# Kernel optimization log

Hardware: AMD Instinct MI355X
Metric: run time of the kernel (lower is better)

The kernel has to match this reference:

```python
import jax, jax.numpy as jnp
import numpy as np

T, D, H, N = 2048, 2048, 32, 64
DW, DA, DV, DG = 64, 64, 32, 128


def _ln(x, w, b, eps):
    mu = x.mean(-1, keepdims=True)
    var = ((x - mu) ** 2).mean(-1, keepdims=True)
    return (x - mu) * jax.lax.rsqrt(var + eps) * w + b


def setup_inputs() -> dict:
    key = jax.random.key(0)
    ks = iter(jax.random.split(key, 40))

    def rn(shape, s=0.02):
        return jax.random.normal(next(ks), shape, dtype=jnp.float32) * s

    def ru(shape):
        return jax.random.uniform(next(ks), shape, dtype=jnp.float32)

    return dict(
        x=rn((T, D), 1.0),
        state1=rn((1, D), 1.0),
        state2=rn((H, N, N), 0.1),
        v_first=rn((T, D), 1.0),
        ln1_w=jnp.ones((D,), jnp.float32),
        ln1_b=jnp.zeros((D,), jnp.float32),
        x_r=ru((D,)), x_w=ru((D,)), x_k=ru((D,)),
        x_v=ru((D,)), x_a=ru((D,)), x_g=ru((D,)),
        W_r=rn((D, D)), W_k=rn((D, D)), W_v=rn((D, D)), W_o=rn((D, D)),
        w1=rn((D, DW)), w2=rn((DW, D)), w0=rn((D,), 0.5),
        a1=rn((D, DA)), a2=rn((DA, D)), a0=rn((D,), 0.5),
        v1=rn((D, DV)), v2=rn((DV, D)), v0=rn((D,), 0.5),
        g1=rn((D, DG)), g2=rn((DG, D)),
        k_k=rn((D,), 0.5), k_a=rn((D,), 0.5), r_k=rn((D,), 0.5),
        ln_x_w=jnp.ones((D,), jnp.float32),
        ln_x_b=jnp.zeros((D,), jnp.float32),
    )


def reference(x, state1, state2, v_first, ln1_w, ln1_b,
              x_r, x_w, x_k, x_v, x_a, x_g,
              W_r, W_k, W_v, W_o,
              w1, w2, w0, a1, a2, a0, v1, v2, v0, g1, g2,
              k_k, k_a, r_k, ln_x_w, ln_x_b):
    # ln1 + token shift
    xn = _ln(x, ln1_w, ln1_b, 1e-5)                      # [T, D]
    sx = jnp.concatenate([state1, xn[:-1]], axis=0) - xn  # shifted - x
    xr = xn + sx * x_r
    xw = xn + sx * x_w
    xk = xn + sx * x_k
    xv = xn + sx * x_v
    xa = xn + sx * x_a
    xg = xn + sx * x_g

    r = xr @ W_r.T
    # decay: w = exp(-0.606531 * sigmoid(w0 + tanh(xw@w1)@w2))
    w = jnp.exp(-0.606531 * jax.nn.sigmoid(jnp.tanh(xw @ w1) @ w2 + w0))
    k = xk @ W_k.T
    v = xv @ W_v.T
    a = jax.nn.sigmoid(xa @ a1 @ a2 + a0)
    g = jax.nn.sigmoid(xg @ g1) @ g2
    # layer_id != 0: blend with v_first via v-lora
    v = v + (v_first - v) * jax.nn.sigmoid(xv @ v1 @ v2 + v0)

    kh = (k * k_k).reshape(T, H, N)
    kk = kh / (jnp.linalg.norm(kh, axis=-1, keepdims=True) + 1e-6)  # l2norm per head
    k = k * (1.0 + (a - 1.0) * k_a)

    rh = r.reshape(T, H, N)
    wh = w.reshape(T, H, N)
    khh = k.reshape(T, H, N)
    vh = v.reshape(T, H, N)
    ab = kk * a.reshape(T, H, N)  # b input to wkv

    def step(S, t):
        r_t, w_t, k_t, v_t, kk_t, ab_t = t
        sa = jnp.einsum('hij,hj->hi', S, -kk_t)  # state @ a (a = -kk column)
        S = (S * w_t[:, None, :]
             + sa[:, :, None] * ab_t[:, None, :]
             + v_t[:, :, None] * k_t[:, None, :])
        return S, jnp.einsum('hij,hj->hi', S, r_t)

    state2_out, xo = jax.lax.scan(step, state2, (rh, wh, khh, vh, kk, ab))  # xo: [T,H,N]

    # per-head layernorm (ln_x, eps=0.00064), then full-width affine
    xo = _ln(xo, jnp.float32(1.0), jnp.float32(0.0), 0.00064)
    xo = xo.reshape(T, D) * ln_x_w + ln_x_b
    # r_k bonus term
    bonus = ((rh * khh * r_k.reshape(H, N)).sum(-1, keepdims=True) * vh).reshape(T, D)
    xo = (xo + bonus) * g
    out = x + xo @ W_o.T
    return out, xn[-1:], state2_out
```

## Files before the change

### kernel.cpp

```cpp
#include <hip/hip_runtime.h>

#define Tn 2048
#define Dn 2048
#define Hn 32
#define Cn 32
#define NCH (Tn / Cn)

typedef float f32x4 __attribute__((ext_vector_type(4)));
typedef __bf16 bf16x8 __attribute__((ext_vector_type(8)));
typedef __bf16 bf16x4 __attribute__((ext_vector_type(4)));

template <int CTRL>
__device__ __forceinline__ float dpp_add(float x) {
  int xi = __builtin_bit_cast(int, x);
  int sh = __builtin_amdgcn_update_dpp(0, xi, CTRL, 0xf, 0xf, true);
  return x + __builtin_bit_cast(float, sh);
}
__device__ __forceinline__ float rdlane(float x, int l) {
  int xi = __builtin_bit_cast(int, x);
  return __builtin_bit_cast(float, __builtin_amdgcn_readlane(xi, l));
}
__device__ __forceinline__ float waveSum(float v) {
  v = dpp_add<0x111>(v);
  v = dpp_add<0x112>(v);
  v = dpp_add<0x114>(v);
  v = dpp_add<0x118>(v);
  return (rdlane(v, 15) + rdlane(v, 31)) + (rdlane(v, 47) + rdlane(v, 63));
}

__device__ __forceinline__ float sigm(float x) { return 1.f / (1.f + expf(-x)); }

__device__ __forceinline__ void gl_lds16(const void* g, void* l) {
  __builtin_amdgcn_global_load_lds(
      (__attribute__((address_space(1))) void*)(g),
      (__attribute__((address_space(3))) void*)(l), 16, 0, 0);
}

__device__ __forceinline__ void bar_lgkm() {
  asm volatile("s_waitcnt lgkmcnt(0)" ::: "memory");
  __builtin_amdgcn_s_barrier();
}

__device__ __forceinline__ f32x4 mfma16(const __bf16* a, const __bf16* b, f32x4 acc) {
  return __builtin_amdgcn_mfma_f32_16x16x32_bf16(
      *(const bf16x8*)a, *(const bf16x8*)b, acc, 0, 0, 0);
}


__global__ __launch_bounds__(256) void castw3_kernel(
    const float* __restrict__ A, const float* __restrict__ B,
    const float* __restrict__ C, __bf16* __restrict__ o0,
    __bf16* __restrict__ o1, __bf16* __restrict__ o2) {
  const int z = blockIdx.y;
  const float* src = z == 0 ? A : (z == 1 ? B : C);
  __bf16* dst = z == 0 ? o0 : (z == 1 ? o1 : o2);
  const size_t i4 = (size_t)blockIdx.x * 256 + threadIdx.x;
  f32x4 v = *(const f32x4*)(src + i4 * 4);
  bf16x4 o;
  o[0] = (__bf16)v[0]; o[1] = (__bf16)v[1]; o[2] = (__bf16)v[2]; o[3] = (__bf16)v[3];
  ((bf16x4*)dst)[i4] = o;
}

__global__ __launch_bounds__(256) void cast1_kernel(
    const float* __restrict__ src, __bf16* __restrict__ dst) {
  const size_t i4 = (size_t)blockIdx.x * 256 + threadIdx.x;
  f32x4 v = *(const f32x4*)(src + i4 * 4);
  bf16x4 o;
  o[0] = (__bf16)v[0]; o[1] = (__bf16)v[1]; o[2] = (__bf16)v[2]; o[3] = (__bf16)v[3];
  ((bf16x4*)dst)[i4] = o;
}

__global__ __launch_bounds__(256) void castT_kernel(
    const float* __restrict__ w2, const float* __restrict__ a2,
    const float* __restrict__ v2, const float* __restrict__ g2,
    __bf16* __restrict__ w2T, __bf16* __restrict__ a2T,
    __bf16* __restrict__ v2T, __bf16* __restrict__ g2T) {
  const int i = blockIdx.x;
  const int k = threadIdx.x;
  if (k < 128) {
    w2T[(size_t)i * 128 + k] = (k < 64) ? (__bf16)w2[(size_t)k * Dn + i] : (__bf16)0.f;
    a2T[(size_t)i * 128 + k] = (k < 64) ? (__bf16)a2[(size_t)k * Dn + i] : (__bf16)0.f;
    v2T[(size_t)i * 128 + k] = (k < 32) ? (__bf16)v2[(size_t)k * Dn + i] : (__bf16)0.f;
    g2T[(size_t)i * 128 + k] = (__bf16)g2[(size_t)k * Dn + i];
  }
}

__global__ __launch_bounds__(256) void castU_kernel(
    const float* __restrict__ w1, const float* __restrict__ a1,
    const float* __restrict__ v1, const float* __restrict__ g1,
    __bf16* __restrict__ uwT, __bf16* __restrict__ uaT,
    __bf16* __restrict__ uvT, __bf16* __restrict__ ugT) {
  const int z = blockIdx.y;
  const float* src = z == 0 ? w1 : (z == 1 ? a1 : (z == 2 ? v1 : g1));
  __bf16* dst = z == 0 ? uwT : (z == 1 ? uaT : (z == 2 ? uvT : ugT));
  const int R = z == 0 ? 64 : (z == 1 ? 64 : (z == 2 ? 32 : 128));
  const int d = blockIdx.x;
  const int k = threadIdx.x;
  if (k < 128)
    dst[(size_t)k * Dn + d] = (k < R) ? (__bf16)src[(size_t)d * R + k] : (__bf16)0.f;
}


__global__ __launch_bounds__(256) void ln_kernel(
    const float* __restrict__ x, const float* __restrict__ lw,
    const float* __restrict__ lb, __bf16* __restrict__ xn,
    float* __restrict__ xn_last) {
  __shared__ float red[8];
  const int t = blockIdx.x, tid = threadIdx.x;
  const int lane = tid & 63, wv = tid >> 6;
  const float* xr = x + (size_t)t * Dn;
  float v[8];
  float s = 0.f;
#pragma unroll
  for (int c = 0; c < 8; ++c) { v[c] = xr[tid + c * 256]; s += v[c]; }
  s = waveSum(s);
  if (lane == 0) red[wv] = s;
  __syncthreads();
  const float mu = (red[0] + red[1] + red[2] + red[3]) * (1.f / (float)Dn);
  float q = 0.f;
#pragma unroll
  for (int c = 0; c < 8; ++c) { float d0 = v[c] - mu; q += d0 * d0; }
  q = waveSum(q);
  if (lane == 0) red[4 + wv] = q;
  __syncthreads();
  const float var = (red[4] + red[5] + red[6] + red[7]) * (1.f / (float)Dn);
  const float rstd = rsqrtf(var + 1e-5f);
#pragma unroll
  for (int c = 0; c < 8; ++c) {
    const int d = tid + c * 256;
    const float y = (v[c] - mu) * rstd * lw[d] + lb[d];
    xn[(size_t)t * Dn + d] = (__bf16)y;
    if (t == Tn - 1) xn_last[d] = y;
  }
}


__global__ __launch_bounds__(256) void mix_kernel(
    const __bf16* __restrict__ xn, const float* __restrict__ state1,
    const float* __restrict__ cr, const float* __restrict__ cw,
    const float* __restrict__ ck, const float* __restrict__ cv,
    const float* __restrict__ ca, const float* __restrict__ cg,
    __bf16* __restrict__ br, __bf16* __restrict__ bw, __bf16* __restrict__ bk,
    __bf16* __restrict__ bv, __bf16* __restrict__ ba, __bf16* __restrict__ bg) {
  const size_t i4 = (size_t)blockIdx.x * 256 + threadIdx.x;
  const int t = (int)(i4 >> 9);
  const int d = (int)(i4 & 511) * 4;
  const bf16x4 cb = ((const bf16x4*)xn)[i4];
  f32x4 cur;
#pragma unroll
  for (int e = 0; e < 4; ++e) cur[e] = (float)cb[e];
  f32x4 prv;
  if (t == 0) {
    prv = *(const f32x4*)(state1 + d);
  } else {
    const bf16x4 pb = ((const bf16x4*)xn)[i4 - 512];
#pragma unroll
    for (int e = 0; e < 4; ++e) prv[e] = (float)pb[e];
  }
  const f32x4 sx = prv - cur;
  auto mix1 = [&](const float* c, __bf16* o) {
    const f32x4 cc = *(const f32x4*)(c + d);
    bf16x4 ob;
#pragma unroll
    for (int e = 0; e < 4; ++e) ob[e] = (__bf16)(cur[e] + sx[e] * cc[e]);
    ((bf16x4*)o)[i4] = ob;
  };
  mix1(cr, br); mix1(cw, bw); mix1(ck, bk);
  mix1(cv, bv); mix1(ca, ba); mix1(cg, bg);
}


__device__ __forceinline__ void gemm_tile(const __bf16* __restrict__ A,
                                          const __bf16* __restrict__ B,
                                          int K, int row0, int col0,
                                          f32x4 (&acc)[4][4]) {
  __shared__ __attribute__((aligned(16))) __bf16 As[4096];
  __shared__ __attribute__((aligned(16))) __bf16 Bs[4096];
  const int tid = threadIdx.x;
  const int lane = tid & 63, wid = tid >> 6;
  const int wm = (wid >> 1) * 64, wn = (wid & 1) * 64;
  const int lr = lane & 15, lk = (lane >> 4) * 8;
  for (int kt = 0; kt < K; kt += 32) {
#pragma unroll
    for (int it = 0; it < 2; ++it) {
      const int L = it * 256 + tid;
      const int rr = L >> 2, kc = (L & 3) * 8;
      const int lb = (it * 256 + wid * 64) * 8;
      gl_lds16(A + (size_t)(row0 + rr) * K + (kt + kc), &As[lb]);
      gl_lds16(B + (size_t)(col0 + rr) * K + (kt + kc), &Bs[lb]);
    }
    __syncthreads();
    bf16x8 af[4], bfv[4];
#pragma unroll
    for (int mf = 0; mf < 4; ++mf)
      af[mf] = *(const bf16x8*)&As[(wm + mf * 16 + lr) * 32 + lk];
#pragma unroll
    for (int nf = 0; nf < 4; ++nf)
      bfv[nf] = *(const bf16x8*)&Bs[(wn + nf * 16 + lr) * 32 + lk];
#pragma unroll
    for (int mf = 0; mf < 4; ++mf)
#pragma unroll
      for (int nf = 0; nf < 4; ++nf)
        acc[mf][nf] = __builtin_amdgcn_mfma_f32_16x16x32_bf16(
            af[mf], bfv[nf], acc[mf][nf], 0, 0, 0);
    __syncthreads();
  }
}

__global__ __launch_bounds__(256) void gemm3_kernel(
    const __bf16* __restrict__ A0, const __bf16* __restrict__ A1,
    const __bf16* __restrict__ A2, const __bf16* __restrict__ B0,
    const __bf16* __restrict__ B1, const __bf16* __restrict__ B2,
    __bf16* __restrict__ C0, __bf16* __restrict__ C1, __bf16* __restrict__ C2) {
  const int z = blockIdx.z;
  const __bf16* A = z == 0 ? A0 : (z == 1 ? A1 : A2);
  const __bf16* B = z == 0 ? B0 : (z == 1 ? B1 : B2);
  __bf16* C = z == 0 ? C0 : (z == 1 ? C1 : C2);
  const int row0 = blockIdx.x * 128, col0 = blockIdx.y * 128;
  f32x4 acc[4][4] = {};
  gemm_tile(A, B, Dn, row0, col0, acc);
  const int lane = threadIdx.x & 63, wid = threadIdx.x >> 6;
  const int wm = (wid >> 1) * 64, wn = (wid & 1) * 64;
#pragma unroll
  for (int mf = 0; mf < 4; ++mf) {
    const int r0 = row0 + wm + mf * 16 + ((lane >> 4) << 2);
#pragma unroll
    for (int nf = 0; nf < 4; ++nf) {
      const int c0 = col0 + wn + nf * 16 + (lane & 15);
#pragma unroll
      for (int rg = 0; rg < 4; ++rg)
        C[(size_t)(r0 + rg) * Dn + c0] = (__bf16)acc[mf][nf][rg];
    }
  }
}

__global__ __launch_bounds__(256) void gemm_l1_kernel(
    const __bf16* __restrict__ Aw, const __bf16* __restrict__ Aa,
    const __bf16* __restrict__ Av, const __bf16* __restrict__ Ag,
    const __bf16* __restrict__ Bw, const __bf16* __restrict__ Ba,
    const __bf16* __restrict__ Bv, const __bf16* __restrict__ Bg,
    __bf16* __restrict__ Cw, __bf16* __restrict__ Ca,
    __bf16* __restrict__ Cv, __bf16* __restrict__ Cg) {
  const int z = blockIdx.z;
  const __bf16* A = z == 0 ? Aw : (z == 1 ? Aa : (z == 2 ? Av : Ag));
  const __bf16* B = z == 0 ? Bw : (z == 1 ? Ba : (z == 2 ? Bv : Bg));
  __bf16* C = z == 0 ? Cw : (z == 1 ? Ca : (z == 2 ? Cv : Cg));
  const int row0 = blockIdx.x * 128;
  f32x4 acc[4][4] = {};
  gemm_tile(A, B, Dn, row0, 0, acc);
  const int lane = threadIdx.x & 63, wid = threadIdx.x >> 6;
  const int wm = (wid >> 1) * 64, wn = (wid & 1) * 64;
#pragma unroll
  for (int mf = 0; mf < 4; ++mf) {
    const int r0 = row0 + wm + mf * 16 + ((lane >> 4) << 2);
#pragma unroll
    for (int nf = 0; nf < 4; ++nf) {
      const int c0 = wn + nf * 16 + (lane & 15);
#pragma unroll
      for (int rg = 0; rg < 4; ++rg) {
        float val = acc[mf][nf][rg];
        if (z == 0)      val = tanhf(val);
        else if (z == 3) val = sigm(val);
        C[(size_t)(r0 + rg) * 128 + c0] = (__bf16)val;
      }
    }
  }
}

__global__ __launch_bounds__(256) void gemm_s2_kernel(
    const __bf16* __restrict__ Aw, const __bf16* __restrict__ Aa,
    const __bf16* __restrict__ Av, const __bf16* __restrict__ Ag,
    const __bf16* __restrict__ Bw, const __bf16* __restrict__ Ba,
    const __bf16* __restrict__ Bv, const __bf16* __restrict__ Bg,
    const float* __restrict__ w0, const float* __restrict__ a0,
    const float* __restrict__ v0, __bf16* __restrict__ Cw,
    __bf16* __restrict__ Ca, __bf16* __restrict__ Cv, __bf16* __restrict__ Cg) {
  const int z = blockIdx.z;
  const __bf16* A = z == 0 ? Aw : (z == 1 ? Aa : (z == 2 ? Av : Ag));
  const __bf16* B = z == 0 ? Bw : (z == 1 ? Ba : (z == 2 ? Bv : Bg));
  const float* bias = z == 0 ? w0 : (z == 1 ? a0 : (z == 2 ? v0 : (const float*)0));
  __bf16* C = z == 0 ? Cw : (z == 1 ? Ca : (z == 2 ? Cv : Cg));
  const int row0 = blockIdx.x * 128, col0 = blockIdx.y * 128;
  f32x4 acc[4][4] = {};
  gemm_tile(A, B, 128, row0, col0, acc);
  const int lane = threadIdx.x & 63, wid = threadIdx.x >> 6;
  const int wm = (wid >> 1) * 64, wn = (wid & 1) * 64;
#pragma unroll
  for (int mf = 0; mf < 4; ++mf) {
    const int r0 = row0 + wm + mf * 16 + ((lane >> 4) << 2);
#pragma unroll
    for (int nf = 0; nf < 4; ++nf) {
      const int c0 = col0 + wn + nf * 16 + (lane & 15);
#pragma unroll
      for (int rg = 0; rg < 4; ++rg) {
        float val = acc[mf][nf][rg];
        if (z == 0)      val = expf(-0.606531f * sigm(val + bias[c0]));
        else if (z < 3)  val = sigm(val + bias[c0]);
        C[(size_t)(r0 + rg) * Dn + c0] = (__bf16)val;
      }
    }
  }
}

__global__ __launch_bounds__(256) void gemm_wo_kernel(
    const __bf16* __restrict__ A, const __bf16* __restrict__ B,
    const float* __restrict__ xres, float* __restrict__ C) {
  const int row0 = blockIdx.x * 128, col0 = blockIdx.y * 128;
  f32x4 acc[4][4] = {};
  gemm_tile(A, B, Dn, row0, col0, acc);
  const int lane = threadIdx.x & 63, wid = threadIdx.x >> 6;
  const int wm = (wid >> 1) * 64, wn = (wid & 1) * 64;
#pragma unroll
  for (int mf = 0; mf < 4; ++mf) {
    const int r0 = row0 + wm + mf * 16 + ((lane >> 4) << 2);
#pragma unroll
    for (int nf = 0; nf < 4; ++nf) {
      const int c0 = col0 + wn + nf * 16 + (lane & 15);
#pragma unroll
      for (int rg = 0; rg < 4; ++rg)
        C[(size_t)(r0 + rg) * Dn + c0] =
            acc[mf][nf][rg] + xres[(size_t)(r0 + rg) * Dn + c0];
    }
  }
}


__global__ __launch_bounds__(256) void prep_kernel(
    const __bf16* __restrict__ r, __bf16* __restrict__ k, __bf16* __restrict__ v,
    const __bf16* __restrict__ a, const __bf16* __restrict__ vb,
    const float* __restrict__ v_first, const float* __restrict__ k_k,
    const float* __restrict__ k_a, const float* __restrict__ r_k,
    __bf16* __restrict__ kk_out, __bf16* __restrict__ ab_out,
    float* __restrict__ dot_out) {
  const int t = blockIdx.x;
  const int lane = threadIdx.x & 63, wv = threadIdx.x >> 6;
#pragma unroll 1
  for (int c = 0; c < 8; ++c) {
    const int d = c * 256 + wv * 64 + lane;
    const size_t idx = (size_t)t * Dn + d;
    const float kvv = (float)k[idx];
    const float kh = kvv * k_k[d];
    const float nrm = sqrtf(waveSum(kh * kh)) + 1e-6f;
    const float kkv = kh / nrm;
    const float av = (float)a[idx];
    float vv = (float)v[idx];
    vv = vv + (v_first[idx] - vv) * (float)vb[idx];
    const float kfv = kvv * (1.f + (av - 1.f) * k_a[d]);
    const float dt = waveSum((float)r[idx] * kfv * r_k[d]);
    kk_out[idx] = (__bf16)kkv;
    ab_out[idx] = (__bf16)(kkv * av);
    k[idx] = (__bf16)kfv;
    v[idx] = (__bf16)vv;
    if (lane == 0) dot_out[t * Hn + (d >> 6)] = dt;
  }
}


__global__ __launch_bounds__(256) void chunkA_kernel(
    const __bf16* __restrict__ wd, const __bf16* __restrict__ kk,
    const __bf16* __restrict__ ab, const __bf16* __restrict__ kf,
    const __bf16* __restrict__ r,
    __bf16* __restrict__ Atil, __bf16* __restrict__ Rtil,
    __bf16* __restrict__ BhatT, __bf16* __restrict__ KhatT,
    __bf16* __restrict__ Pg, __bf16* __restrict__ PKg,
    __bf16* __restrict__ Gbg, __bf16* __restrict__ Gkg,
    float* __restrict__ WCg) {
  const int c = blockIdx.x, h = blockIdx.y;
  const int tid = threadIdx.x;
  __shared__ __bf16 A_l[32][72];
  __shared__ __bf16 B_l[32][72], K_l[32][72], R_l[32][72];
  __shared__ float W_l[33][64];
  __shared__ float Mba[32][36], Mka[32][36];
  __shared__ float P0[32][36], P1[32][36], T0[32][36], T1[32][36];

  const size_t rowbase = (size_t)(c * Cn) * Dn + (size_t)h * 64;
  const int tt = tid >> 3, j0 = (tid & 7) * 8;
  const size_t g = rowbase + (size_t)tt * Dn + j0;
  *(bf16x8*)&A_l[tt][j0] = *(const bf16x8*)(wd + g);
  __syncthreads();
  if (tid < 64) {
    const int j = tid;
    float cur = 1.f;
    W_l[0][j] = 1.f;
    for (int t = 0; t < Cn; ++t) {
      cur *= (float)A_l[t][j];
      W_l[t + 1][j] = cur;
    }
    WCg[((size_t)c * Hn + h) * 64 + j] = cur;
  }
  __syncthreads();
  {
    bf16x8 kkv = *(const bf16x8*)(kk + g);
    bf16x8 abv = *(const bf16x8*)(ab + g);
    bf16x8 kv  = *(const bf16x8*)(kf + g);
    bf16x8 rv  = *(const bf16x8*)(r + g);
    bf16x8 oa, ob, ok, orr;
    const size_t tb = ((size_t)c * Hn + h) * 2048;
#pragma unroll
    for (int e = 0; e < 8; ++e) {
      const int j = j0 + e;
      const float Wexc = W_l[tt][j], Winc = W_l[tt + 1][j], WC = W_l[32][j];
      const float inv = 1.f / Winc;
      const float at = -(float)kkv[e] * Wexc;
      const float bt = (float)abv[e] * inv;
      const float kt = (float)kv[e] * inv;
      const float rt = (float)rv[e] * Winc;
      oa[e] = (__bf16)at; ob[e] = (__bf16)bt; ok[e] = (__bf16)kt;
      orr[e] = (__bf16)rt;
      BhatT[tb + (size_t)j * 32 + tt] = (__bf16)(bt * WC);
      KhatT[tb + (size_t)j * 32 + tt] = (__bf16)(kt * WC);
    }
    *(bf16x8*)&A_l[tt][j0] = oa;
    *(bf16x8*)&B_l[tt][j0] = ob;
    *(bf16x8*)&K_l[tt][j0] = ok;
    *(bf16x8*)&R_l[tt][j0] = orr;
    *(bf16x8*)(Atil + g) = oa;
    *(bf16x8*)(Rtil + g) = orr;
  }
  __syncthreads();
  const size_t matbase = ((size_t)c * Hn + h) * (Cn * Cn);
#pragma unroll 1
  for (int rep = 0; rep < 4; ++rep) {
    const int id = rep * 256 + tid;
    const int t = id >> 5, ta = id & 31;
    float d_ab = 0.f, d_ak = 0.f, d_rb = 0.f, d_rk = 0.f;
    for (int j8 = 0; j8 < 8; ++j8) {
      const bf16x8 av = *(const bf16x8*)&A_l[t][j8 * 8];
      const bf16x8 rv = *(const bf16x8*)&R_l[t][j8 * 8];
      const bf16x8 bv = *(const bf16x8*)&B_l[ta][j8 * 8];
      const bf16x8 kv = *(const bf16x8*)&K_l[ta][j8 * 8];
#pragma unroll
      for (int e = 0; e < 8; ++e) {
        const float af = (float)av[e], rf = (float)rv[e];
        const float bf2 = (float)bv[e], kf2 = (float)kv[e];
        d_ab += af * bf2; d_ak += af * kf2;
        d_rb += rf * bf2; d_rk += rf * kf2;
      }
    }
    Mba[t][ta] = (ta < t) ? d_ab : 0.f;
    Mka[t][ta] = (ta < t) ? d_ak : 0.f;
    Gbg[matbase + id] = (__bf16)((ta <= t) ? d_rb : 0.f);
    Gkg[matbase + id] = (__bf16)((ta <= t) ? d_rk : 0.f);
  }
  __syncthreads();
  for (int rep = 0; rep < 4; ++rep) {
    const int id = rep * 256 + tid;
    const int t = id >> 5, ta = id & 31;
    P0[t][ta] = Mba[t][ta] + (t == ta ? 1.f : 0.f);
  }
  __syncthreads();
  auto mm = [&](float (*D)[36], float (*Aa)[36], float (*Bb)[36]) {
    for (int rep = 0; rep < 4; ++rep) {
      const int id = rep * 256 + tid;
      const int t = id >> 5, ta = id & 31;
      float s = 0.f;
      for (int u = 0; u < 32; ++u) s += Aa[t][u] * Bb[u][ta];
      D[t][ta] = s;
    }
    __syncthreads();
  };
  auto mmadd = [&](float (*D)[36], float (*Pp)[36], float (*Tt)[36]) {
    for (int rep = 0; rep < 4; ++rep) {
      const int id = rep * 256 + tid;
      const int t = id >> 5, ta = id & 31;
      float s = Pp[t][ta];
      for (int u = 0; u < 32; ++u) s += Pp[t][u] * Tt[u][ta];
      D[t][ta] = s;
    }
    __syncthreads();
  };
  mm(T0, Mba, Mba);
  mmadd(P1, P0, T0);
  mm(T1, T0, T0);
  mmadd(P0, P1, T1);
  mm(T0, T1, T1);
  mmadd(P1, P0, T0);
  mm(T1, T0, T0);
  mmadd(P0, P1, T1);
  for (int rep = 0; rep < 4; ++rep) {
    const int id = rep * 256 + tid;
    const int t = id >> 5, ta = id & 31;
    Pg[matbase + id] = (__bf16)P0[t][ta];
    float s = 0.f;
    for (int u = 0; u < 32; ++u) s += P0[t][u] * Mka[u][ta];
    PKg[matbase + id] = (__bf16)s;
  }
}


__global__ __launch_bounds__(256) void vt_kernel(
    const __bf16* __restrict__ vbuf, __bf16* __restrict__ Vt) {
  const int c = blockIdx.x, h = blockIdx.y;
  __shared__ __bf16 tile[32][72];
  const int tid = threadIdx.x;
  {
    const int t = tid >> 3, i0 = (tid & 7) * 8;
    *(bf16x8*)&tile[t][i0] =
        *(const bf16x8*)(vbuf + (size_t)(c * Cn + t) * Dn + h * 64 + i0);
  }
  __syncthreads();
  {
    const int i = tid >> 2, t0 = (tid & 3) * 8;
    bf16x8 o;
#pragma unroll
    for (int e = 0; e < 8; ++e) o[e] = tile[t0 + e][i];
    *(bf16x8*)(Vt + ((size_t)c * Hn + h) * 2048 + (size_t)i * 32 + t0) = o;
  }
}


__global__ __launch_bounds__(256) void chunkB_kernel(
    const __bf16* __restrict__ Atil, const __bf16* __restrict__ Rtil,
    const __bf16* __restrict__ BhatT, const __bf16* __restrict__ KhatT,
    const __bf16* __restrict__ Pg, const __bf16* __restrict__ PKg,
    const __bf16* __restrict__ Gbg, const __bf16* __restrict__ Gkg,
    const float* __restrict__ WCg, const __bf16* __restrict__ Vt,
    const float* __restrict__ st_in, __bf16* __restrict__ xo,
    float* __restrict__ st_out) {
  const int b = blockIdx.x;
  const int xcd = b & 7, rest = b >> 3;
  const int h = xcd * 4 + (rest & 3);
  const int io = (rest >> 2) * 32;
  const int tid = threadIdx.x;
  const int lane = tid & 63, wid = tid >> 6;
  const int lr = lane & 15, lg = lane >> 4;
  const int lk = lg * 8;

  __shared__ __attribute__((aligned(16))) float S_l[32][68];
  __shared__ __attribute__((aligned(16))) __bf16 Sb_l[32][72];
  __shared__ __attribute__((aligned(16))) __bf16 A_l[32][72], R_l[32][72];
  __shared__ __attribute__((aligned(16))) __bf16 BhT_l[64][40], KhT_l[64][40];
  __shared__ __attribute__((aligned(16))) __bf16 Vt_l[32][40];
  __shared__ __attribute__((aligned(16))) __bf16 P_l[32][40], PK_l[32][40];
  __shared__ __attribute__((aligned(16))) __bf16 Gb_l[32][40], Gk_l[32][40];
  __shared__ __attribute__((aligned(16))) __bf16 X_l[32][40], SA_l[32][40];
  __shared__ float WC_l[64];

  {
    const int i = tid >> 3, j0 = (tid & 7) * 8;
    const float* src = st_in + (size_t)h * 4096 + (size_t)(io + i) * 64 + j0;
    *(f32x4*)&S_l[i][j0] = *(const f32x4*)src;
    *(f32x4*)&S_l[i][j0 + 4] = *(const f32x4*)(src + 4);
  }

  bf16x8 rA, rR, rBh, rKh;
  bf16x4 rV, rP, rPK, rGb, rGk;
  float rWC = 0.f;

  auto load_regs = [&](int c) {
    const size_t rb = (size_t)(c * Cn) * Dn + (size_t)h * 64;
    {
      const int t = tid >> 3, j0 = (tid & 7) * 8;
      rA = *(const bf16x8*)(Atil + rb + (size_t)t * Dn + j0);
      rR = *(const bf16x8*)(Rtil + rb + (size_t)t * Dn + j0);
    }
    const size_t tb = ((size_t)c * Hn + h) * 2048;
    {
      const int jj = tid >> 2, t0 = (tid & 3) * 8;
      rBh = *(const bf16x8*)(BhatT + tb + (size_t)jj * 32 + t0);
      rKh = *(const bf16x8*)(KhatT + tb + (size_t)jj * 32 + t0);
    }
    {
      const int i = tid >> 3, t0 = (tid & 7) * 4;
      rV = *(const bf16x4*)(Vt + tb + (size_t)(io + i) * 32 + t0);
    }
    const size_t mb = ((size_t)c * Hn + h) * 1024 + (size_t)tid * 4;
    rP  = *(const bf16x4*)(Pg + mb);
    rPK = *(const bf16x4*)(PKg + mb);
    rGb = *(const bf16x4*)(Gbg + mb);
    rGk = *(const bf16x4*)(Gkg + mb);
    if (tid < 64) rWC = WCg[((size_t)c * Hn + h) * 64 + tid];
  };
  auto store_lds = [&]() {
    {
      const int t = tid >> 3, j0 = (tid & 7) * 8;
      *(bf16x8*)&A_l[t][j0] = rA;
      *(bf16x8*)&R_l[t][j0] = rR;
    }
    {
      const int jj = tid >> 2, t0 = (tid & 3) * 8;
      *(bf16x8*)&BhT_l[jj][t0] = rBh;
      *(bf16x8*)&KhT_l[jj][t0] = rKh;
    }
    {
      const int i = tid >> 3, t0 = (tid & 7) * 4;
      *(bf16x4*)&Vt_l[i][t0] = rV;
    }
    {
      const int t = tid >> 3, u0 = (tid & 7) * 4;
      *(bf16x4*)&P_l[t][u0] = rP;
      *(bf16x4*)&PK_l[t][u0] = rPK;
      *(bf16x4*)&Gb_l[t][u0] = rGb;
      *(bf16x4*)&Gk_l[t][u0] = rGk;
    }
    if (tid < 64) WC_l[tid] = rWC;
  };
  auto sb_refresh = [&]() {
    const int i = tid >> 3, j0 = (tid & 7) * 8;
    bf16x8 o;
#pragma unroll
    for (int e = 0; e < 8; ++e) o[e] = (__bf16)S_l[i][j0 + e];
    *(bf16x8*)&Sb_l[i][j0] = o;
  };

  load_regs(0);
  store_lds();
  sb_refresh();
  bar_lgkm();

  const int tm = (wid >> 1) * 16, tn = (wid & 1) * 16;

#pragma unroll 1
  for (int c = 0; c < NCH; ++c) {
    load_regs(c + 1 < NCH ? c + 1 : c);
    {
      f32x4 acc = {};
      acc = mfma16(&A_l[tm + lr][lk], &Sb_l[tn + lr][lk], acc);
      acc = mfma16(&A_l[tm + lr][32 + lk], &Sb_l[tn + lr][32 + lk], acc);
      bf16x4 o;
#pragma unroll
      for (int e = 0; e < 4; ++e) o[e] = (__bf16)acc[e];
      *(bf16x4*)&X_l[tn + lr][tm + lg * 4] = o;
    }
    bar_lgkm();
    {
      f32x4 acc = {};
      acc = mfma16(&P_l[tm + lr][lk], &X_l[tn + lr][lk], acc);
      acc = mfma16(&PK_l[tm + lr][lk], &Vt_l[tn + lr][lk], acc);
      bf16x4 o;
#pragma unroll
      for (int e = 0; e < 4; ++e) o[e] = (__bf16)acc[e];
      *(bf16x4*)&SA_l[tn + lr][tm + lg * 4] = o;
    }
    bar_lgkm();
    {
      f32x4 acc = {};
      acc = mfma16(&Gb_l[tm + lr][lk], &SA_l[tn + lr][lk], acc);
      acc = mfma16(&Gk_l[tm + lr][lk], &Vt_l[tn + lr][lk], acc);
      acc = mfma16(&R_l[tm + lr][lk], &Sb_l[tn + lr][lk], acc);
      acc = mfma16(&R_l[tm + lr][32 + lk], &Sb_l[tn + lr][32 + lk], acc);
      const int ig = h * 64 + io + tn + lr;
#pragma unroll
      for (int e = 0; e < 4; ++e)
        xo[(size_t)(c * Cn + tm + lg * 4 + e) * Dn + ig] = (__bf16)acc[e];
    }
#pragma unroll
    for (int tt = 0; tt < 2; ++tt) {
      const int tix = wid + tt * 4;
      const int im = (tix & 1) * 16, jn = (tix >> 1) * 16;
      const float wc = WC_l[jn + lr];
      f32x4 acc;
#pragma unroll
      for (int e = 0; e < 4; ++e) acc[e] = S_l[im + lg * 4 + e][jn + lr] * wc;
      acc = mfma16(&SA_l[im + lr][lk], &BhT_l[jn + lr][lk], acc);
      acc = mfma16(&Vt_l[im + lr][lk], &KhT_l[jn + lr][lk], acc);
#pragma unroll
      for (int e = 0; e < 4; ++e) S_l[im + lg * 4 + e][jn + lr] = acc[e];
    }
    bar_lgkm();
    store_lds();
    sb_refresh();
    bar_lgkm();
  }
  {
    const int i = tid >> 3, j0 = (tid & 7) * 8;
    float* dst = st_out + (size_t)h * 4096 + (size_t)(io + i) * 64 + j0;
    *(f32x4*)dst = *(const f32x4*)&S_l[i][j0];
    *(f32x4*)(dst + 4) = *(const f32x4*)&S_l[i][j0 + 4];
  }
}


__global__ __launch_bounds__(256) void post_kernel(
    const __bf16* __restrict__ xo, const __bf16* __restrict__ v,
    const __bf16* __restrict__ g, const float* __restrict__ dot,
    const float* __restrict__ lnw, const float* __restrict__ lnb,
    __bf16* __restrict__ out) {
  const int t = blockIdx.x;
  const int lane = threadIdx.x & 63, wv = threadIdx.x >> 6;
#pragma unroll 1
  for (int c = 0; c < 8; ++c) {
    const int d = c * 256 + wv * 64 + lane;
    const size_t idx = (size_t)t * Dn + d;
    const float val = (float)xo[idx];
    const float mu = waveSum(val) * (1.f / 64.f);
    const float ctr = val - mu;
    const float var = waveSum(ctr * ctr) * (1.f / 64.f);
    float y = ctr * rsqrtf(var + 0.00064f);
    y = y * lnw[d] + lnb[d];
    const float res = (y + dot[t * Hn + (d >> 6)] * (float)v[idx]) * (float)g[idx];
    out[idx] = (__bf16)res;
  }
}


extern "C" void kernel_launch(void* const* d_in, const int* in_sizes, int n_in,
                              void* d_out, int out_size, void* d_ws, size_t ws_size,
                              hipStream_t stream) {
  (void)in_sizes; (void)n_in; (void)out_size; (void)ws_size;
  const float* x       = (const float*)d_in[0];
  const float* state1  = (const float*)d_in[1];
  const float* state2  = (const float*)d_in[2];
  const float* v_first = (const float*)d_in[3];
  const float* ln1_w   = (const float*)d_in[4];
  const float* ln1_b   = (const float*)d_in[5];
  const float* x_r     = (const float*)d_in[6];
  const float* x_w     = (const float*)d_in[7];
  const float* x_k     = (const float*)d_in[8];
  const float* x_v     = (const float*)d_in[9];
  const float* x_a     = (const float*)d_in[10];
  const float* x_g     = (const float*)d_in[11];
  const float* W_r     = (const float*)d_in[12];
  const float* W_k     = (const float*)d_in[13];
  const float* W_v     = (const float*)d_in[14];
  const float* W_o     = (const float*)d_in[15];
  const float* w1      = (const float*)d_in[16];
  const float* w2      = (const float*)d_in[17];
  const float* w0      = (const float*)d_in[18];
  const float* a1      = (const float*)d_in[19];
  const float* a2      = (const float*)d_in[20];
  const float* a0      = (const float*)d_in[21];
  const float* v1      = (const float*)d_in[22];
  const float* v2      = (const float*)d_in[23];
  const float* v0      = (const float*)d_in[24];
  const float* g1      = (const float*)d_in[25];
  const float* g2      = (const float*)d_in[26];
  const float* k_k     = (const float*)d_in[27];
  const float* k_a     = (const float*)d_in[28];
  const float* r_k     = (const float*)d_in[29];
  const float* lnx_w   = (const float*)d_in[30];
  const float* lnx_b   = (const float*)d_in[31];

  char* p = (char*)d_ws;
  const size_t MB = 1ull << 20;
  __bf16* xn    = (__bf16*)(p + 0 * MB);
  __bf16* Atil  = (__bf16*)(p + 0 * MB);
  __bf16* xr_b  = (__bf16*)(p + 8 * MB);
  __bf16* Wo_b  = (__bf16*)(p + 8 * MB);
  __bf16* xw_b  = (__bf16*)(p + 16 * MB);
  __bf16* wdec  = (__bf16*)(p + 16 * MB);
  __bf16* xo_b  = (__bf16*)(p + 16 * MB);
  __bf16* xk_b  = (__bf16*)(p + 24 * MB);
  __bf16* abuf  = (__bf16*)(p + 24 * MB);
  __bf16* Rtil  = (__bf16*)(p + 24 * MB);
  __bf16* xv_b  = (__bf16*)(p + 32 * MB);
  __bf16* vbl   = (__bf16*)(p + 32 * MB);
  __bf16* BhatT = (__bf16*)(p + 32 * MB);
  __bf16* xa_b  = (__bf16*)(p + 40 * MB);
  __bf16* gbuf  = (__bf16*)(p + 40 * MB);
  __bf16* xg_b  = (__bf16*)(p + 48 * MB);
  __bf16* kkbuf = (__bf16*)(p + 48 * MB);
  __bf16* xobuf = (__bf16*)(p + 48 * MB);
  __bf16* Wr_b  = (__bf16*)(p + 56 * MB);
  __bf16* abbuf = (__bf16*)(p + 56 * MB);
  __bf16* Wk_b  = (__bf16*)(p + 64 * MB);
  __bf16* KhatT = (__bf16*)(p + 64 * MB);
  __bf16* Wv_b  = (__bf16*)(p + 72 * MB);
  __bf16* Pg    = (__bf16*)(p + 72 * MB);
  __bf16* PKg   = (__bf16*)(p + 76 * MB);
  __bf16* rbuf  = (__bf16*)(p + 80 * MB);
  __bf16* kbuf  = (__bf16*)(p + 88 * MB);
  __bf16* Vt    = (__bf16*)(p + 88 * MB);
  __bf16* vbuf  = (__bf16*)(p + 96 * MB);
  __bf16* Gbg   = (__bf16*)(p + 104 * MB);
  __bf16* Gkg   = (__bf16*)(p + 108 * MB);
  char* q = p + 112 * MB;
  __bf16* yw  = (__bf16*)q; q += (size_t)Tn * 128 * 2;
  __bf16* ya  = (__bf16*)q; q += (size_t)Tn * 128 * 2;
  __bf16* yv  = (__bf16*)q; q += (size_t)Tn * 128 * 2;
  __bf16* yg  = (__bf16*)q; q += (size_t)Tn * 128 * 2;
  __bf16* uwT = (__bf16*)q; q += (size_t)128 * Dn * 2;
  __bf16* uaT = (__bf16*)q; q += (size_t)128 * Dn * 2;
  __bf16* uvT = (__bf16*)q; q += (size_t)128 * Dn * 2;
  __bf16* ugT = (__bf16*)q; q += (size_t)128 * Dn * 2;
  __bf16* w2T = (__bf16*)q; q += (size_t)Dn * 128 * 2;
  __bf16* a2T = (__bf16*)q; q += (size_t)Dn * 128 * 2;
  __bf16* v2T = (__bf16*)q; q += (size_t)Dn * 128 * 2;
  __bf16* g2T = (__bf16*)q; q += (size_t)Dn * 128 * 2;
  float*  dot = (float*)q;  q += (size_t)Tn * Hn * 4;
  float*  WCg = (float*)q;  q += (size_t)NCH * Hn * 64 * 4;

  float* out     = (float*)d_out;
  float* out_xnl = out + (size_t)Tn * Dn;
  float* out_st  = out_xnl + Dn;

  castw3_kernel<<<dim3(4096, 3), 256, 0, stream>>>(W_r, W_k, W_v, Wr_b, Wk_b, Wv_b);
  castT_kernel<<<2048, 256, 0, stream>>>(w2, a2, v2, g2, w2T, a2T, v2T, g2T);
  castU_kernel<<<dim3(2048, 4), 256, 0, stream>>>(w1, a1, v1, g1, uwT, uaT, uvT, ugT);
  ln_kernel<<<2048, 256, 0, stream>>>(x, ln1_w, ln1_b, xn, out_xnl);
  mix_kernel<<<4096, 256, 0, stream>>>(xn, state1, x_r, x_w, x_k, x_v, x_a, x_g,
                                       xr_b, xw_b, xk_b, xv_b, xa_b, xg_b);
  gemm3_kernel<<<dim3(16, 16, 3), 256, 0, stream>>>(
      xr_b, xk_b, xv_b, Wr_b, Wk_b, Wv_b, rbuf, kbuf, vbuf);
  cast1_kernel<<<4096, 256, 0, stream>>>(W_o, Wo_b);
  gemm_l1_kernel<<<dim3(16, 1, 4), 256, 0, stream>>>(
      xw_b, xa_b, xv_b, xg_b, uwT, uaT, uvT, ugT, yw, ya, yv, yg);
  gemm_s2_kernel<<<dim3(16, 16, 4), 256, 0, stream>>>(
      yw, ya, yv, yg, w2T, a2T, v2T, g2T, w0, a0, v0, wdec, abuf, vbl, gbuf);
  prep_kernel<<<2048, 256, 0, stream>>>(rbuf, kbuf, vbuf, abuf, vbl, v_first,
                                        k_k, k_a, r_k, kkbuf, abbuf, dot);
  chunkA_kernel<<<dim3(NCH, Hn), 256, 0, stream>>>(
      wdec, kkbuf, abbuf, kbuf, rbuf,
      Atil, Rtil, BhatT, KhatT, Pg, PKg, Gbg, Gkg, WCg);
  vt_kernel<<<dim3(NCH, Hn), 256, 0, stream>>>(vbuf, Vt);
  chunkB_kernel<<<64, 256, 0, stream>>>(
      Atil, Rtil, BhatT, KhatT, Pg, PKg, Gbg, Gkg, WCg, Vt,
      state2, xobuf, out_st);
  post_kernel<<<2048, 256, 0, stream>>>(xobuf, vbuf, gbuf, dot, lnx_w, lnx_b, xo_b);
  gemm_wo_kernel<<<dim3(16, 16), 256, 0, stream>>>(xo_b, Wo_b, x, out);
}
```

Baseline: 428.1 us.

## Precompute P·A per chunk in chunkA and merge the big and LoRA GEMM launches

```diff
diff --git a/kernel.cpp b/kernel.cpp
--- a/kernel.cpp
+++ b/kernel.cpp
@@ -207,34 +207,11 @@
   }
 }
 
-__global__ __launch_bounds__(256) void gemm3_kernel(
+__global__ __launch_bounds__(256) void gemm37_kernel(
     const __bf16* __restrict__ A0, const __bf16* __restrict__ A1,
     const __bf16* __restrict__ A2, const __bf16* __restrict__ B0,
     const __bf16* __restrict__ B1, const __bf16* __restrict__ B2,
-    __bf16* __restrict__ C0, __bf16* __restrict__ C1, __bf16* __restrict__ C2) {
-  const int z = blockIdx.z;
-  const __bf16* A = z == 0 ? A0 : (z == 1 ? A1 : A2);
-  const __bf16* B = z == 0 ? B0 : (z == 1 ? B1 : B2);
-  __bf16* C = z == 0 ? C0 : (z == 1 ? C1 : C2);
-  const int row0 = blockIdx.x * 128, col0 = blockIdx.y * 128;
-  f32x4 acc[4][4] = {};
-  gemm_tile(A, B, Dn, row0, col0, acc);
-  const int lane = threadIdx.x & 63, wid = threadIdx.x >> 6;
-  const int wm = (wid >> 1) * 64, wn = (wid & 1) * 64;
-#pragma unroll
-  for (int mf = 0; mf < 4; ++mf) {
-    const int r0 = row0 + wm + mf * 16 + ((lane >> 4) << 2);
-#pragma unroll
-    for (int nf = 0; nf < 4; ++nf) {
-      const int c0 = col0 + wn + nf * 16 + (lane & 15);
-#pragma unroll
-      for (int rg = 0; rg < 4; ++rg)
-        C[(size_t)(r0 + rg) * Dn + c0] = (__bf16)acc[mf][nf][rg];
-    }
-  }
-}
-
-__global__ __launch_bounds__(256) void gemm_l1_kernel(
+    __bf16* __restrict__ C0, __bf16* __restrict__ C1, __bf16* __restrict__ C2,
     const __bf16* __restrict__ Aw, const __bf16* __restrict__ Aa,
     const __bf16* __restrict__ Av, const __bf16* __restrict__ Ag,
     const __bf16* __restrict__ Bw, const __bf16* __restrict__ Ba,
@@ -242,12 +219,21 @@
     __bf16* __restrict__ Cw, __bf16* __restrict__ Ca,
     __bf16* __restrict__ Cv, __bf16* __restrict__ Cg) {
   const int z = blockIdx.z;
-  const __bf16* A = z == 0 ? Aw : (z == 1 ? Aa : (z == 2 ? Av : Ag));
-  const __bf16* B = z == 0 ? Bw : (z == 1 ? Ba : (z == 2 ? Bv : Bg));
-  __bf16* C = z == 0 ? Cw : (z == 1 ? Ca : (z == 2 ? Cv : Cg));
-  const int row0 = blockIdx.x * 128;
+  if (z >= 3 && blockIdx.y != 0) return;
+  const __bf16* A; const __bf16* B; __bf16* C;
+  switch (z) {
+    case 0: A = A0; B = B0; C = C0; break;
+    case 1: A = A1; B = B1; C = C1; break;
+    case 2: A = A2; B = B2; C = C2; break;
+    case 3: A = Aw; B = Bw; C = Cw; break;
+    case 4: A = Aa; B = Ba; C = Ca; break;
+    case 5: A = Av; B = Bv; C = Cv; break;
+    default: A = Ag; B = Bg; C = Cg; break;
+  }
+  const int row0 = blockIdx.x * 128, col0 = (z < 3) ? blockIdx.y * 128 : 0;
+  const int ldc = (z < 3) ? Dn : 128;
   f32x4 acc[4][4] = {};
-  gemm_tile(A, B, Dn, row0, 0, acc);
+  gemm_tile(A, B, Dn, row0, col0, acc);
   const int lane = threadIdx.x & 63, wid = threadIdx.x >> 6;
   const int wm = (wid >> 1) * 64, wn = (wid & 1) * 64;
 #pragma unroll
@@ -255,13 +241,13 @@
     const int r0 = row0 + wm + mf * 16 + ((lane >> 4) << 2);
 #pragma unroll
     for (int nf = 0; nf < 4; ++nf) {
-      const int c0 = wn + nf * 16 + (lane & 15);
+      const int c0 = col0 + wn + nf * 16 + (lane & 15);
 #pragma unroll
       for (int rg = 0; rg < 4; ++rg) {
         float val = acc[mf][nf][rg];
-        if (z == 0)      val = tanhf(val);
-        else if (z == 3) val = sigm(val);
-        C[(size_t)(r0 + rg) * 128 + c0] = (__bf16)val;
+        if (z == 3)      val = tanhf(val);
+        else if (z == 6) val = sigm(val);
+        C[(size_t)(r0 + rg) * ldc + c0] = (__bf16)val;
       }
     }
   }
@@ -360,9 +346,9 @@
     const __bf16* __restrict__ wd, const __bf16* __restrict__ kk,
     const __bf16* __restrict__ ab, const __bf16* __restrict__ kf,
     const __bf16* __restrict__ r,
-    __bf16* __restrict__ Atil, __bf16* __restrict__ Rtil,
+    __bf16* __restrict__ PAg, __bf16* __restrict__ Rtil,
     __bf16* __restrict__ BhatT, __bf16* __restrict__ KhatT,
-    __bf16* __restrict__ Pg, __bf16* __restrict__ PKg,
+    __bf16* __restrict__ PKg,
     __bf16* __restrict__ Gbg, __bf16* __restrict__ Gkg,
     float* __restrict__ WCg) {
   const int c = blockIdx.x, h = blockIdx.y;
@@ -414,7 +400,6 @@
     *(bf16x8*)&B_l[tt][j0] = ob;
     *(bf16x8*)&K_l[tt][j0] = ok;
     *(bf16x8*)&R_l[tt][j0] = orr;
-    *(bf16x8*)(Atil + g) = oa;
     *(bf16x8*)(Rtil + g) = orr;
   }
   __syncthreads();
@@ -480,10 +465,16 @@
   for (int rep = 0; rep < 4; ++rep) {
     const int id = rep * 256 + tid;
     const int t = id >> 5, ta = id & 31;
-    Pg[matbase + id] = (__bf16)P0[t][ta];
     float s = 0.f;
     for (int u = 0; u < 32; ++u) s += P0[t][u] * Mka[u][ta];
     PKg[matbase + id] = (__bf16)s;
+  }
+  for (int rep = 0; rep < 8; ++rep) {
+    const int id = rep * 256 + tid;
+    const int t = id >> 6, j = id & 63;
+    float s = 0.f;
+    for (int u = 0; u < 32; ++u) s += P0[t][u] * (float)A_l[u][j];
+    PAg[rowbase + (size_t)t * Dn + j] = (__bf16)s;
   }
 }
 
@@ -510,9 +501,9 @@
 
 
 __global__ __launch_bounds__(256) void chunkB_kernel(
-    const __bf16* __restrict__ Atil, const __bf16* __restrict__ Rtil,
+    const __bf16* __restrict__ PAg, const __bf16* __restrict__ Rtil,
     const __bf16* __restrict__ BhatT, const __bf16* __restrict__ KhatT,
-    const __bf16* __restrict__ Pg, const __bf16* __restrict__ PKg,
+    const __bf16* __restrict__ PKg,
     const __bf16* __restrict__ Gbg, const __bf16* __restrict__ Gkg,
     const float* __restrict__ WCg, const __bf16* __restrict__ Vt,
     const float* __restrict__ st_in, __bf16* __restrict__ xo,
@@ -528,12 +519,12 @@
 
   __shared__ __attribute__((aligned(16))) float S_l[32][68];
   __shared__ __attribute__((aligned(16))) __bf16 Sb_l[32][72];
-  __shared__ __attribute__((aligned(16))) __bf16 A_l[32][72], R_l[32][72];
+  __shared__ __attribute__((aligned(16))) __bf16 PA_l[32][72], R_l[32][72];
   __shared__ __attribute__((aligned(16))) __bf16 BhT_l[64][40], KhT_l[64][40];
   __shared__ __attribute__((aligned(16))) __bf16 Vt_l[32][40];
-  __shared__ __attribute__((aligned(16))) __bf16 P_l[32][40], PK_l[32][40];
+  __shared__ __attribute__((aligned(16))) __bf16 PK_l[32][40];
   __shared__ __attribute__((aligned(16))) __bf16 Gb_l[32][40], Gk_l[32][40];
-  __shared__ __attribute__((aligned(16))) __bf16 X_l[32][40], SA_l[32][40];
+  __shared__ __attribute__((aligned(16))) __bf16 SA_l[32][40];
   __shared__ float WC_l[64];
 
   {
@@ -543,16 +534,16 @@
     *(f32x4*)&S_l[i][j0 + 4] = *(const f32x4*)(src + 4);
   }
 
-  bf16x8 rA, rR, rBh, rKh;
-  bf16x4 rV, rP, rPK, rGb, rGk;
+  bf16x8 rPA, rR, rBh, rKh;
+  bf16x4 rV, rPK, rGb, rGk;
   float rWC = 0.f;
 
   auto load_regs = [&](int c) {
     const size_t rb = (size_t)(c * Cn) * Dn + (size_t)h * 64;
     {
       const int t = tid >> 3, j0 = (tid & 7) * 8;
-      rA = *(const bf16x8*)(Atil + rb + (size_t)t * Dn + j0);
-      rR = *(const bf16x8*)(Rtil + rb + (size_t)t * Dn + j0);
+      rPA = *(const bf16x8*)(PAg + rb + (size_t)t * Dn + j0);
+      rR  = *(const bf16x8*)(Rtil + rb + (size_t)t * Dn + j0);
     }
     const size_t tb = ((size_t)c * Hn + h) * 2048;
     {
@@ -565,7 +556,6 @@
       rV = *(const bf16x4*)(Vt + tb + (size_t)(io + i) * 32 + t0);
     }
     const size_t mb = ((size_t)c * Hn + h) * 1024 + (size_t)tid * 4;
-    rP  = *(const bf16x4*)(Pg + mb);
     rPK = *(const bf16x4*)(PKg + mb);
     rGb = *(const bf16x4*)(Gbg + mb);
     rGk = *(const bf16x4*)(Gkg + mb);
@@ -574,7 +564,7 @@
   auto store_lds = [&]() {
     {
       const int t = tid >> 3, j0 = (tid & 7) * 8;
-      *(bf16x8*)&A_l[t][j0] = rA;
+      *(bf16x8*)&PA_l[t][j0] = rPA;
       *(bf16x8*)&R_l[t][j0] = rR;
     }
     {
@@ -588,7 +578,6 @@
     }
     {
       const int t = tid >> 3, u0 = (tid & 7) * 4;
-      *(bf16x4*)&P_l[t][u0] = rP;
       *(bf16x4*)&PK_l[t][u0] = rPK;
       *(bf16x4*)&Gb_l[t][u0] = rGb;
       *(bf16x4*)&Gk_l[t][u0] = rGk;
@@ -615,17 +604,8 @@
     load_regs(c + 1 < NCH ? c + 1 : c);
     {
       f32x4 acc = {};
-      acc = mfma16(&A_l[tm + lr][lk], &Sb_l[tn + lr][lk], acc);
-      acc = mfma16(&A_l[tm + lr][32 + lk], &Sb_l[tn + lr][32 + lk], acc);
-      bf16x4 o;
-#pragma unroll
-      for (int e = 0; e < 4; ++e) o[e] = (__bf16)acc[e];
-      *(bf16x4*)&X_l[tn + lr][tm + lg * 4] = o;
-    }
-    bar_lgkm();
-    {
-      f32x4 acc = {};
-      acc = mfma16(&P_l[tm + lr][lk], &X_l[tn + lr][lk], acc);
+      acc = mfma16(&PA_l[tm + lr][lk], &Sb_l[tn + lr][lk], acc);
+      acc = mfma16(&PA_l[tm + lr][32 + lk], &Sb_l[tn + lr][32 + lk], acc);
       acc = mfma16(&PK_l[tm + lr][lk], &Vt_l[tn + lr][lk], acc);
       bf16x4 o;
 #pragma unroll
@@ -734,7 +714,7 @@
   char* p = (char*)d_ws;
   const size_t MB = 1ull << 20;
   __bf16* xn    = (__bf16*)(p + 0 * MB);
-  __bf16* Atil  = (__bf16*)(p + 0 * MB);
+  __bf16* PAg   = (__bf16*)(p + 0 * MB);
   __bf16* xr_b  = (__bf16*)(p + 8 * MB);
   __bf16* Wo_b  = (__bf16*)(p + 8 * MB);
   __bf16* xw_b  = (__bf16*)(p + 16 * MB);
@@ -756,8 +736,7 @@
   __bf16* Wk_b  = (__bf16*)(p + 64 * MB);
   __bf16* KhatT = (__bf16*)(p + 64 * MB);
   __bf16* Wv_b  = (__bf16*)(p + 72 * MB);
-  __bf16* Pg    = (__bf16*)(p + 72 * MB);
-  __bf16* PKg   = (__bf16*)(p + 76 * MB);
+  __bf16* PKg   = (__bf16*)(p + 72 * MB);
   __bf16* rbuf  = (__bf16*)(p + 80 * MB);
   __bf16* kbuf  = (__bf16*)(p + 88 * MB);
   __bf16* Vt    = (__bf16*)(p + 88 * MB);
@@ -790,21 +769,20 @@
   ln_kernel<<<2048, 256, 0, stream>>>(x, ln1_w, ln1_b, xn, out_xnl);
   mix_kernel<<<4096, 256, 0, stream>>>(xn, state1, x_r, x_w, x_k, x_v, x_a, x_g,
                                        xr_b, xw_b, xk_b, xv_b, xa_b, xg_b);
-  gemm3_kernel<<<dim3(16, 16, 3), 256, 0, stream>>>(
-      xr_b, xk_b, xv_b, Wr_b, Wk_b, Wv_b, rbuf, kbuf, vbuf);
+  gemm37_kernel<<<dim3(16, 16, 7), 256, 0, stream>>>(
+      xr_b, xk_b, xv_b, Wr_b, Wk_b, Wv_b, rbuf, kbuf, vbuf,
+      xw_b, xa_b, xv_b, xg_b, uwT, uaT, uvT, ugT, yw, ya, yv, yg);
   cast1_kernel<<<4096, 256, 0, stream>>>(W_o, Wo_b);
-  gemm_l1_kernel<<<dim3(16, 1, 4), 256, 0, stream>>>(
-      xw_b, xa_b, xv_b, xg_b, uwT, uaT, uvT, ugT, yw, ya, yv, yg);
   gemm_s2_kernel<<<dim3(16, 16, 4), 256, 0, stream>>>(
       yw, ya, yv, yg, w2T, a2T, v2T, g2T, w0, a0, v0, wdec, abuf, vbl, gbuf);
   prep_kernel<<<2048, 256, 0, stream>>>(rbuf, kbuf, vbuf, abuf, vbl, v_first,
                                         k_k, k_a, r_k, kkbuf, abbuf, dot);
   chunkA_kernel<<<dim3(NCH, Hn), 256, 0, stream>>>(
       wdec, kkbuf, abbuf, kbuf, rbuf,
-      Atil, Rtil, BhatT, KhatT, Pg, PKg, Gbg, Gkg, WCg);
+      PAg, Rtil, BhatT, KhatT, PKg, Gbg, Gkg, WCg);
   vt_kernel<<<dim3(NCH, Hn), 256, 0, stream>>>(vbuf, Vt);
   chunkB_kernel<<<64, 256, 0, stream>>>(
-      Atil, Rtil, BhatT, KhatT, Pg, PKg, Gbg, Gkg, WCg, Vt,
+      PAg, Rtil, BhatT, KhatT, PKg, Gbg, Gkg, WCg, Vt,
       state2, xobuf, out_st);
   post_kernel<<<2048, 256, 0, stream>>>(xobuf, vbuf, gbuf, dot, lnx_w, lnx_b, xo_b);
   gemm_wo_kernel<<<dim3(16, 16), 256, 0, stream>>>(xo_b, Wo_b, x, out);
```

After: 483.6 us. 13.0% more time.
